# Kernel tuning notes

Measured on AMD Instinct MI355X. Metric: run time of the kernel, lower is better.

## Reference

```python
import jax, jax.numpy as jnp
import numpy as np

B, LATENT, P, NUM_ATOMS, H, L, E = 16, 128, 16, 64, 64, 4, 32768
N = P * NUM_ATOMS  # 1024

def _lin(k, i, o, s=0.05):
    kw, kb = jax.random.split(k)
    return jax.random.normal(kw, (i, o), jnp.float32) * s, jax.random.normal(kb, (o,), jnp.float32) * s

def setup_inputs() -> dict:
    key = jax.random.key(0)
    ks = jax.random.split(key, 32)
    z = jax.random.normal(ks[0], (B, LATENT), jnp.float32)
    edge_index = jax.random.randint(ks[1], (2, E), 0, N, jnp.int32)
    # build_node_features: (frame/P, atom/num_atoms, 1) per node
    fr = jnp.repeat(jnp.arange(P), NUM_ATOMS) / P
    at = jnp.tile(jnp.arange(NUM_ATOMS), P) / NUM_ATOMS
    node_features = jnp.stack([fr, at, jnp.ones(N)], -1).astype(jnp.float32)
    Wg, bg = _lin(ks[2], LATENT, H)
    Wn, bn = _lin(ks[3], 3, H)
    def stack(fn, base):
        outs = [fn(jax.random.fold_in(key, base + l)) for l in range(L)]
        return tuple(jnp.stack(t) for t in zip(*outs))
    eW1, eb1 = stack(lambda k: _lin(k, 2 * H + 1, H), 100)
    eW2, eb2 = stack(lambda k: _lin(k, H, H), 200)
    cW1, cb1 = stack(lambda k: _lin(k, H, H), 300)
    cW2 = jnp.stack([jax.random.normal(jax.random.fold_in(key, 400 + l), (H, 1), jnp.float32) * 0.05 for l in range(L)])
    nW1, nb1 = stack(lambda k: _lin(k, 2 * H, H), 500)
    nW2, nb2 = stack(lambda k: _lin(k, H, H), 600)
    lng = jnp.ones((L, H), jnp.float32)
    lnb = jnp.zeros((L, H), jnp.float32)
    oW1, ob1 = _lin(ks[4], H, H)
    oW2, ob2 = _lin(ks[5], H, 3)
    return dict(z=z, edge_index=edge_index, node_features=node_features, Wg=Wg, bg=bg, Wn=Wn, bn=bn,
                eW1=eW1, eb1=eb1, eW2=eW2, eb2=eb2, cW1=cW1, cb1=cb1, cW2=cW2,
                nW1=nW1, nb1=nb1, nW2=nW2, nb2=nb2, lng=lng, lnb=lnb,
                oW1=oW1, ob1=ob1, oW2=oW2, ob2=ob2)

def _forward(z, edge_index, node_features, Wg, bg, Wn, bn, eW1, eb1, eW2, eb2,
             cW1, cb1, cW2, nW1, nb1, nW2, nb2, lng, lnb, oW1, ob1, oW2, ob2):
    b = z.shape[0]
    n = node_features.shape[0]
    row, col = edge_index[0], edge_index[1]  # aggregate messages to row
    counts = jnp.clip(jnp.zeros((n,), jnp.float32).at[row].add(1.0), 1.0, None)
    g = z @ Wg + bg                              # [B,H]
    h = (node_features @ Wn + bn)[None] + g[:, None]  # [B,N,H]
    pos = jnp.zeros((b, n, 3), h.dtype)
    for l in range(L):
        hi, hj = h[:, row], h[:, col]            # [B,E,H] gathers
        diff = pos[:, row] - pos[:, col]         # [B,E,3]
        d2 = jnp.sum(diff * diff, -1, keepdims=True)
        m = jax.nn.silu(jnp.concatenate([hi, hj, d2], -1) @ eW1[l] + eb1[l])
        m = jax.nn.silu(m @ eW2[l] + eb2[l])     # [B,E,H]
        w = jax.nn.silu(m @ cW1[l] + cb1[l]) @ cW2[l]  # [B,E,1]
        trans = diff * w
        pos = pos + jnp.zeros_like(pos).at[:, row].add(trans) / counts[None, :, None]
        agg = jnp.zeros_like(h).at[:, row].add(m)      # scatter-sum to nodes
        u = jax.nn.silu(jnp.concatenate([h, agg], -1) @ nW1[l] + nb1[l]) @ nW2[l] + nb2[l]
        h = h + u                                 # node residual
        mu = jnp.mean(h, -1, keepdims=True)
        var = jnp.mean((h - mu) ** 2, -1, keepdims=True)
        h = (h - mu) * jax.lax.rsqrt(var + 1e-5) * lng[l] + lnb[l]
    out = jax.nn.relu(h @ oW1 + ob1) @ oW2 + ob2   # [B,N,3]
    return out.reshape(b, -1)

def reference(z, edge_index, node_features, Wg, bg, Wn, bn, eW1, eb1, eW2, eb2,
              cW1, cb1, cW2, nW1, nb1, nW2, nb2, lng, lnb, oW1, ob1, oW2, ob2):
    return _forward(z, edge_index, node_features, Wg, bg, Wn, bn, eW1, eb1, eW2, eb2,
                    cW1, cb1, cW2, nW1, nb1, nW2, nb2, lng, lnb, oW1, ob1, oW2, ob2)
```

## Files before the change

kernel.cpp:

```cpp
#include <hip/hip_runtime.h>
#include <hip/hip_bf16.h>


namespace {

constexpr int kE = 32768, kLat = 128;

typedef __attribute__((ext_vector_type(8))) short short8;
typedef __attribute__((ext_vector_type(4))) float floatx4;

__device__ __forceinline__ unsigned short f2bf(float f){
  union { float f; unsigned int u; } v; v.f = f;
  unsigned int r = v.u + 0x7fffu + ((v.u >> 16) & 1u);
  return (unsigned short)(r >> 16);
}
__device__ __forceinline__ unsigned int packbf(float a, float b){
  return ((unsigned int)f2bf(b) << 16) | (unsigned int)f2bf(a);
}
__device__ __forceinline__ unsigned int pack2f(float a, float b){
  unsigned int ua = __float_as_uint(a) + 0x8000u;
  unsigned int ub = __float_as_uint(b) + 0x8000u;
  return __builtin_amdgcn_perm(ub, ua, 0x07060302);
}
__device__ __forceinline__ float bflo(unsigned int u){
  union { unsigned int u; float f; } v; v.u = u << 16; return v.f;
}
__device__ __forceinline__ float bfhi(unsigned int u){
  union { unsigned int u; float f; } v; v.u = u & 0xffff0000u; return v.f;
}
__device__ __forceinline__ float silu2(float x){
  float u = __builtin_amdgcn_exp2f(-1.44269504f * x);
  return x * __builtin_amdgcn_rcpf(1.0f + u);
}

__device__ __forceinline__ void stage16k(float* Wl, const float* src, int tid){
  const float4* p = (const float4*)src;
  float4* d = (float4*)Wl;
  d[tid]       = p[tid];
  d[tid + 256] = p[tid + 256];
  d[tid + 512] = p[tid + 512];
  d[tid + 768] = p[tid + 768];
}
__device__ __forceinline__ void xtwrite(float* XTl, int j0, int r0,
                                        const float v[4][4]){
  #pragma unroll
  for (int j = 0; j < 4; j++){
    float4 t = { v[0][j], v[1][j], v[2][j], v[3][j] };
    *(float4*)(XTl + (j0 + j)*68 + r0) = t;
  }
}
__device__ __forceinline__ void gemm64(const float* Wl, const float* XTl,
                                       int j0, int r0, float acc[4][4]){
  #pragma unroll 4
  for (int k = 0; k < 64; k++){
    float4 w = *(const float4*)(Wl + k*64 + j0);
    float4 x = *(const float4*)(XTl + k*68 + r0);
    float xv[4] = { x.x, x.y, x.z, x.w };
    float wv[4] = { w.x, w.y, w.z, w.w };
    #pragma unroll
    for (int i = 0; i < 4; i++)
      #pragma unroll
      for (int j = 0; j < 4; j++)
        acc[i][j] += xv[i]*wv[j];
  }
}

__global__ void k_scancnt(const int* ei, int* off, int* fill){
  __shared__ int s0[1024];
  __shared__ int s1[1024];
  int t = threadIdx.x;
  s0[t] = 0; fill[t] = 0;
  __syncthreads();
  #pragma unroll
  for (int i = 0; i < 32; i++) atomicAdd(&s0[ei[i*1024 + t]], 1);
  __syncthreads();
  int c = s0[t];
  int* src = s0; int* dst = s1;
  for (int o = 1; o < 1024; o <<= 1){
    int v = src[t] + ((t >= o) ? src[t-o] : 0);
    dst[t] = v; __syncthreads();
    int* tmp = src; src = dst; dst = tmp;
  }
  int inc = src[t];
  off[t] = inc - c;
  if (t == 1023) off[1024] = inc;
}

__global__ void k_bucket(const int* ei, const int* off, int* fill, int* ecol,
                         const float* eW2, unsigned short* wfragE,
                         const float* z, const float* Wg, const float* bg,
                         float* g){
  int e = blockIdx.x*256 + threadIdx.x;
  int r = ei[e];
  int s = atomicAdd(&fill[r], 1);
  ecol[off[r] + s] = ei[kE + e];
  if (blockIdx.x < 4){
    int l = blockIdx.x;
    for (int i = threadIdx.x; i < 4096; i += 256){
      int f = i >> 9, lane = (i >> 3) & 63, j8 = i & 7;
      int jt = f >> 1, ks = f & 1;
      int k = ks*32 + (lane >> 4)*8 + j8;
      int j = jt*16 + (lane & 15);
      wfragE[l*4096 + i] = f2bf(eW2[l*4096 + k*64 + j]);
    }
  } else if (blockIdx.x < 8){
    int b = (blockIdx.x - 4)*4 + (threadIdx.x >> 6);
    int j = threadIdx.x & 63;
    float acc = bg[j];
    for (int k = 0; k < kLat; k++) acc += z[b*kLat + k] * Wg[k*64 + j];
    g[b*64 + j] = acc;
  }
}

__global__ __launch_bounds__(256, 1) void k_preA(const float* nf, const float* Wn,
      const float* bn, const float* g, const float* eW1, const float* eb1,
      float* An1, float* An2, float* Ag1, float* Ag2){
  __shared__ __align__(16) float W0[4096];
  __shared__ __align__(16) float W1[4096];
  __shared__ __align__(16) float HR[16*68];
  int tid = threadIdx.x;
  if (blockIdx.x == 64){
    int bb = tid >> 4, j0 = (tid & 15)*4;
    float a1[4] = {0.f,0.f,0.f,0.f}, a2[4] = {0.f,0.f,0.f,0.f};
    for (int k = 0; k < 64; k++){
      float gk = g[bb*64 + k];
      float4 w1 = *(const float4*)(eW1 + k*64 + j0);
      float4 w2 = *(const float4*)(eW1 + 4096 + k*64 + j0);
      a1[0] += gk*w1.x; a1[1] += gk*w1.y; a1[2] += gk*w1.z; a1[3] += gk*w1.w;
      a2[0] += gk*w2.x; a2[1] += gk*w2.y; a2[2] += gk*w2.z; a2[3] += gk*w2.w;
    }
    float4 o1 = { a1[0], a1[1], a1[2], a1[3] };
    float4 o2 = { a2[0], a2[1], a2[2], a2[3] };
    *(float4*)(Ag1 + bb*64 + j0) = o1;
    *(float4*)(Ag2 + bb*64 + j0) = o2;
    return;
  }
  {
    const float4* e1a = (const float4*)(eW1);
    const float4* e1b = (const float4*)(eW1 + 4096);
    for (int i = tid; i < 1024; i += 256){
      ((float4*)W0)[i] = e1a[i]; ((float4*)W1)[i] = e1b[i];
    }
  }
  int rl = tid >> 4, c = tid & 15, j0 = c*4;
  int n = blockIdx.x*16 + rl;
  float f0 = nf[n*3], f1 = nf[n*3+1], f2 = nf[n*3+2];
  float4 hv;
  hv.x = f0*Wn[j0+0] + f1*Wn[64+j0+0] + f2*Wn[128+j0+0] + bn[j0+0];
  hv.y = f0*Wn[j0+1] + f1*Wn[64+j0+1] + f2*Wn[128+j0+1] + bn[j0+1];
  hv.z = f0*Wn[j0+2] + f1*Wn[64+j0+2] + f2*Wn[128+j0+2] + bn[j0+2];
  hv.w = f0*Wn[j0+3] + f1*Wn[64+j0+3] + f2*Wn[128+j0+3] + bn[j0+3];
  *(float4*)(HR + rl*68 + j0) = hv;
  __syncthreads();
  float4 b1 = *(const float4*)(eb1 + j0);
  float a1[4] = { b1.x, b1.y, b1.z, b1.w };
  float a2[4] = { 0.f, 0.f, 0.f, 0.f };
  #pragma unroll 8
  for (int k = 0; k < 64; k++){
    float hk = HR[rl*68 + k];
    float4 w1 = *(const float4*)(W0 + k*64 + j0);
    float4 w2 = *(const float4*)(W1 + k*64 + j0);
    a1[0] += hk*w1.x; a1[1] += hk*w1.y; a1[2] += hk*w1.z; a1[3] += hk*w1.w;
    a2[0] += hk*w2.x; a2[1] += hk*w2.y; a2[2] += hk*w2.z; a2[3] += hk*w2.w;
  }
  float4 o1 = { a1[0], a1[1], a1[2], a1[3] };
  float4 o2 = { a2[0], a2[1], a2[2], a2[3] };
  *(float4*)(An1 + n*64 + j0) = o1;
  *(float4*)(An2 + n*64 + j0) = o2;
}

__global__ __launch_bounds__(256, 1) void k_pre1(const float* nf, const float* Wn,
      const float* bn, const float* g, const float* An1, const float* An2,
      const float* Ag1, const float* Ag2, float* h, float* A1,
      unsigned short* A2){
  int idx = blockIdx.x*256 + threadIdx.x;
  int row = idx >> 4;
  int j0  = (idx & 15) * 4;
  int n = row >> 4, bb = row & 15;
  float4 a1 = *(const float4*)(An1 + n*64 + j0);
  float4 g1 = *(const float4*)(Ag1 + bb*64 + j0);
  a1.x += g1.x; a1.y += g1.y; a1.z += g1.z; a1.w += g1.w;
  *(float4*)(A1 + row*64 + j0) = a1;
  float4 a2 = *(const float4*)(An2 + n*64 + j0);
  float4 g2 = *(const float4*)(Ag2 + bb*64 + j0);
  a2.x += g2.x; a2.y += g2.y; a2.z += g2.z; a2.w += g2.w;
  uint2 pk; pk.x = packbf(a2.x, a2.y); pk.y = packbf(a2.z, a2.w);
  *(uint2*)(A2 + row*64 + j0) = pk;
  float f0 = nf[n*3], f1 = nf[n*3+1], f2 = nf[n*3+2];
  float4 w0 = *(const float4*)(Wn + j0);
  float4 w1 = *(const float4*)(Wn + 64 + j0);
  float4 w2 = *(const float4*)(Wn + 128 + j0);
  float4 bv = *(const float4*)(bn + j0);
  float4 gv = *(const float4*)(g + bb*64 + j0);
  float4 hv;
  hv.x = f0*w0.x + f1*w1.x + f2*w2.x + bv.x + gv.x;
  hv.y = f0*w0.y + f1*w1.y + f2*w2.y + bv.y + gv.y;
  hv.z = f0*w0.z + f1*w1.z + f2*w2.z + bv.z + gv.z;
  hv.w = f0*w0.w + f1*w1.w + f2*w2.w + bv.w + gv.w;
  *(float4*)(h + (bb*1024 + n)*64 + j0) = hv;
}

template <bool LAST>
__global__ __launch_bounds__(256) void k_layer(int l,
      const float* A1r, const unsigned short* A2r,
      float* A1w, unsigned short* A2w,
      float* h, const unsigned short* wfragE, const float* eb2,
      const int* off, const int* ecol,
      const float* nW1, const float* nb1_, const float* nW2, const float* nb2_,
      const float* lng_, const float* lnb_, const float* eW1, const float* eb1_,
      const float* oW1, const float* ob1_, const float* oW2, const float* ob2_,
      float* out){
  __shared__ __align__(16) float W[4096];
  __shared__ __align__(16) float XT[64*68];
  __shared__ __align__(16) float AGL[64*68];
  __shared__ float W2o[192];
  __shared__ float ob2s[4];
  int tid = threadIdx.x, bid = blockIdx.x;
  int n0 = bid * 4;
  int lane = tid & 63, wv = tid >> 6, m = lane & 15, quad = lane >> 4;

  {
    int nd = n0 + wv;
    short8 wf[8];
    #pragma unroll
    for (int f = 0; f < 8; f++)
      wf[f] = *(const short8*)(wfragE + l*4096 + f*512 + lane*8);
    floatx4 dini[4], agg[4];
    #pragma unroll
    for (int jt = 0; jt < 4; jt++){
      dini[jt] = *(const floatx4*)(eb2 + l*64 + jt*16 + quad*4);
      agg[jt] = (floatx4){0.f,0.f,0.f,0.f};
    }
    int e0 = off[nd], e1 = off[nd+1];
    if (e0 < e1){
      float4 a1[4];
      #pragma unroll
      for (int ks = 0; ks < 2; ks++){
        a1[ks*2+0] = *(const float4*)(A1r + (nd<<10) + (m<<6) + ks*32 + quad*8);
        a1[ks*2+1] = *(const float4*)(A1r + (nd<<10) + (m<<6) + ks*32 + quad*8 + 4);
      }
      int c0 = ecol[e0];
      uint4 p0 = *(const uint4*)(A2r + ((c0<<4)+m)*64 + quad*8);
      uint4 p1 = *(const uint4*)(A2r + ((c0<<4)+m)*64 + 32 + quad*8);
      for (int e = e0; e < e1; e++){
        uint4 c_0 = p0, c_1 = p1;
        if (e + 1 < e1){
          int cn = ecol[e+1];
          p0 = *(const uint4*)(A2r + ((cn<<4)+m)*64 + quad*8);
          p1 = *(const uint4*)(A2r + ((cn<<4)+m)*64 + 32 + quad*8);
        }
        short8 bfr[2];
        #pragma unroll
        for (int ks = 0; ks < 2; ks++){
          uint4 a2r = (ks == 0) ? c_0 : c_1;
          float4 x0 = a1[ks*2+0];
          float4 x1 = a1[ks*2+1];
          float v0 = silu2(x0.x + bflo(a2r.x));
          float v1 = silu2(x0.y + bfhi(a2r.x));
          float v2 = silu2(x0.z + bflo(a2r.y));
          float v3 = silu2(x0.w + bfhi(a2r.y));
          float v4 = silu2(x1.x + bflo(a2r.z));
          float v5 = silu2(x1.y + bfhi(a2r.z));
          float v6 = silu2(x1.z + bflo(a2r.w));
          float v7 = silu2(x1.w + bfhi(a2r.w));
          union { uint4 u; short8 s; } bu;
          bu.u.x = pack2f(v0, v1); bu.u.y = pack2f(v2, v3);
          bu.u.z = pack2f(v4, v5); bu.u.w = pack2f(v6, v7);
          bfr[ks] = bu.s;
        }
        #pragma unroll
        for (int jt = 0; jt < 4; jt++){
          floatx4 d = dini[jt];
          d = __builtin_amdgcn_mfma_f32_16x16x32_bf16(wf[jt*2+0], bfr[0], d, 0, 0, 0);
          d = __builtin_amdgcn_mfma_f32_16x16x32_bf16(wf[jt*2+1], bfr[1], d, 0, 0, 0);
          floatx4 a = agg[jt];
          a.x += silu2(d.x); a.y += silu2(d.y);
          a.z += silu2(d.z); a.w += silu2(d.w);
          agg[jt] = a;
        }
      }
    }
    #pragma unroll
    for (int jt = 0; jt < 4; jt++){
      #pragma unroll
      for (int i = 0; i < 4; i++)
        AGL[(jt*16 + quad*4 + i)*68 + wv*16 + m] = agg[jt][i];
    }
  }

  int c = tid & 15, gq = tid >> 4;
  int j0 = c*4, r0 = gq*4;

  stage16k(W, nW1 + l*8192, tid);
  float hold[4][4];
  #pragma unroll
  for (int i = 0; i < 4; i++){
    int rr = r0 + i;
    int n = n0 + (rr >> 4), bb = rr & 15;
    float4 v = *(const float4*)(h + (bb*1024 + n)*64 + j0);
    hold[i][0]=v.x; hold[i][1]=v.y; hold[i][2]=v.z; hold[i][3]=v.w;
  }
  xtwrite(XT, j0, r0, hold);
  float acc[4][4];
  { float4 b1 = *(const float4*)(nb1_ + l*64 + j0);
    float bv[4] = { b1.x, b1.y, b1.z, b1.w };
    #pragma unroll
    for (int i = 0; i < 4; i++)
      #pragma unroll
      for (int j = 0; j < 4; j++) acc[i][j] = bv[j]; }
  __syncthreads();
  gemm64(W, XT, j0, r0, acc);
  __syncthreads();
  stage16k(W, nW1 + l*8192 + 4096, tid);
  __syncthreads();
  gemm64(W, AGL, j0, r0, acc);
  #pragma unroll
  for (int i = 0; i < 4; i++)
    #pragma unroll
    for (int j = 0; j < 4; j++) acc[i][j] = silu2(acc[i][j]);
  __syncthreads();
  stage16k(W, nW2 + l*4096, tid);
  xtwrite(XT, j0, r0, acc);
  float u[4][4];
  { float4 b2 = *(const float4*)(nb2_ + l*64 + j0);
    float bv[4] = { b2.x, b2.y, b2.z, b2.w };
    #pragma unroll
    for (int i = 0; i < 4; i++)
      #pragma unroll
      for (int j = 0; j < 4; j++) u[i][j] = bv[j]; }
  __syncthreads();
  gemm64(W, XT, j0, r0, u);
  float4 lgv = *(const float4*)(lng_ + l*64 + j0);
  float4 lbv = *(const float4*)(lnb_ + l*64 + j0);
  float hn[4][4];
  #pragma unroll
  for (int i = 0; i < 4; i++){
    float hv[4];
    #pragma unroll
    for (int j = 0; j < 4; j++) hv[j] = hold[i][j] + u[i][j];
    float s1 = hv[0]+hv[1]+hv[2]+hv[3];
    float s2 = hv[0]*hv[0]+hv[1]*hv[1]+hv[2]*hv[2]+hv[3]*hv[3];
    s1 += __shfl_xor(s1, 1, 64); s1 += __shfl_xor(s1, 2, 64);
    s1 += __shfl_xor(s1, 4, 64); s1 += __shfl_xor(s1, 8, 64);
    s2 += __shfl_xor(s2, 1, 64); s2 += __shfl_xor(s2, 2, 64);
    s2 += __shfl_xor(s2, 4, 64); s2 += __shfl_xor(s2, 8, 64);
    float mu  = s1 * (1.0f/64.0f);
    float var = s2 * (1.0f/64.0f) - mu*mu;
    float rs  = rsqrtf(var + 1e-5f);
    hn[i][0] = (hv[0]-mu)*rs*lgv.x + lbv.x;
    hn[i][1] = (hv[1]-mu)*rs*lgv.y + lbv.y;
    hn[i][2] = (hv[2]-mu)*rs*lgv.z + lbv.z;
    hn[i][3] = (hv[3]-mu)*rs*lgv.w + lbv.w;
  }

  if (!LAST){
    #pragma unroll
    for (int i = 0; i < 4; i++){
      int rr = r0 + i;
      int n = n0 + (rr >> 4), bb = rr & 15;
      float4 v = { hn[i][0], hn[i][1], hn[i][2], hn[i][3] };
      *(float4*)(h + (bb*1024 + n)*64 + j0) = v;
    }
    __syncthreads();
    stage16k(W, eW1 + (l+1)*8256, tid);
    xtwrite(XT, j0, r0, hn);
    float a1r[4][4];
    { float4 b1 = *(const float4*)(eb1_ + (l+1)*64 + j0);
      float bv[4] = { b1.x, b1.y, b1.z, b1.w };
      #pragma unroll
      for (int i = 0; i < 4; i++)
        #pragma unroll
        for (int j = 0; j < 4; j++) a1r[i][j] = bv[j]; }
    __syncthreads();
    gemm64(W, XT, j0, r0, a1r);
    __syncthreads();
    stage16k(W, eW1 + (l+1)*8256 + 4096, tid);
    float a2r[4][4];
    #pragma unroll
    for (int i = 0; i < 4; i++)
      #pragma unroll
      for (int j = 0; j < 4; j++) a2r[i][j] = 0.f;
    __syncthreads();
    gemm64(W, XT, j0, r0, a2r);
    #pragma unroll
    for (int i = 0; i < 4; i++){
      int rr = r0 + i;
      int n = n0 + (rr >> 4), bb = rr & 15;
      int tb = (n*16 + bb)*64 + j0;
      float4 o1 = { a1r[i][0], a1r[i][1], a1r[i][2], a1r[i][3] };
      *(float4*)(A1w + tb) = o1;
      uint2 pk; pk.x = packbf(a2r[i][0], a2r[i][1]);
      pk.y = packbf(a2r[i][2], a2r[i][3]);
      *(uint2*)(A2w + tb) = pk;
    }
  } else {
    __syncthreads();
    stage16k(W, oW1, tid);
    if (tid < 192) W2o[tid] = oW2[tid];
    if (tid < 3)   ob2s[tid] = ob2_[tid];
    xtwrite(XT, j0, r0, hn);
    __syncthreads();
    float tr[4][4];
    { float4 b1 = *(const float4*)(ob1_ + j0);
      float bv[4] = { b1.x, b1.y, b1.z, b1.w };
      #pragma unroll
      for (int i = 0; i < 4; i++)
        #pragma unroll
        for (int j = 0; j < 4; j++) tr[i][j] = bv[j]; }
    gemm64(W, XT, j0, r0, tr);
    #pragma unroll
    for (int i = 0; i < 4; i++)
      #pragma unroll
      for (int j = 0; j < 4; j++) tr[i][j] = fmaxf(tr[i][j], 0.f);
    float po[4][3];
    #pragma unroll
    for (int i = 0; i < 4; i++){ po[i][0]=0.f; po[i][1]=0.f; po[i][2]=0.f; }
    #pragma unroll
    for (int j = 0; j < 4; j++){
      float w0 = W2o[(j0+j)*3 + 0];
      float w1 = W2o[(j0+j)*3 + 1];
      float w2 = W2o[(j0+j)*3 + 2];
      #pragma unroll
      for (int i = 0; i < 4; i++){
        po[i][0] += tr[i][j]*w0;
        po[i][1] += tr[i][j]*w1;
        po[i][2] += tr[i][j]*w2;
      }
    }
    #pragma unroll
    for (int i = 0; i < 4; i++)
      #pragma unroll
      for (int uu = 0; uu < 3; uu++){
        float v = po[i][uu];
        v += __shfl_xor(v, 1, 64); v += __shfl_xor(v, 2, 64);
        v += __shfl_xor(v, 4, 64); v += __shfl_xor(v, 8, 64);
        po[i][uu] = v;
      }
    if (c == 0){
      #pragma unroll
      for (int i = 0; i < 4; i++){
        int rr = r0 + i;
        int n = n0 + (rr >> 4), bb = rr & 15;
        out[bb*3072 + n*3 + 0] = po[i][0] + ob2s[0];
        out[bb*3072 + n*3 + 1] = po[i][1] + ob2s[1];
        out[bb*3072 + n*3 + 2] = po[i][2] + ob2s[2];
      }
    }
  }
}

}

extern "C" void kernel_launch(void* const* d_in, const int* in_sizes, int n_in,
                              void* d_out, int out_size, void* d_ws, size_t ws_size,
                              hipStream_t stream){
  const float* z   = (const float*)d_in[0];
  const int*   ei  = (const int*)d_in[1];
  const float* nf  = (const float*)d_in[2];
  const float* Wg  = (const float*)d_in[3];  const float* bg  = (const float*)d_in[4];
  const float* Wn  = (const float*)d_in[5];  const float* bn  = (const float*)d_in[6];
  const float* eW1 = (const float*)d_in[7];  const float* eb1 = (const float*)d_in[8];
  const float* eW2 = (const float*)d_in[9];  const float* eb2 = (const float*)d_in[10];
  const float* nW1 = (const float*)d_in[14]; const float* nb1 = (const float*)d_in[15];
  const float* nW2 = (const float*)d_in[16]; const float* nb2 = (const float*)d_in[17];
  const float* lng = (const float*)d_in[18]; const float* lnb = (const float*)d_in[19];
  const float* oW1 = (const float*)d_in[20]; const float* ob1 = (const float*)d_in[21];
  const float* oW2 = (const float*)d_in[22]; const float* ob2 = (const float*)d_in[23];

  float* W      = (float*)d_ws;
  float* h      = W;
  float* A1a    = W + 1048576;
  float* A1b    = W + 2097152;
  unsigned short* A2a    = (unsigned short*)(W + 3145728);
  unsigned short* A2b    = (unsigned short*)(W + 3670016);
  unsigned short* wfragE = (unsigned short*)(W + 4194304);
  float* g      = W + 4202496;
  float* An1    = W + 4203520;
  float* An2    = W + 4269056;
  float* Ag1    = W + 4334592;
  float* Ag2    = W + 4335616;
  int*   off    = (int*)(W + 4336640);
  int*   fill   = off + 1025;
  int*   ecol   = fill + 1024;

  k_scancnt<<<1, 1024, 0, stream>>>(ei, off, fill);
  k_bucket <<<128, 256, 0, stream>>>(ei, off, fill, ecol, eW2, wfragE, z, Wg, bg, g);
  k_preA   <<<65,  256, 0, stream>>>(nf, Wn, bn, g, eW1, eb1, An1, An2, Ag1, Ag2);
  k_pre1   <<<1024,256, 0, stream>>>(nf, Wn, bn, g, An1, An2, Ag1, Ag2, h, A1a, A2a);

  for (int l = 0; l < 4; l++){
    const float* A1r = (l & 1) ? A1b : A1a;
    const unsigned short* A2r = (l & 1) ? A2b : A2a;
    float* A1w = (l & 1) ? A1a : A1b;
    unsigned short* A2w = (l & 1) ? A2a : A2b;
    if (l < 3)
      k_layer<false><<<256, 256, 0, stream>>>(l, A1r, A2r, A1w, A2w, h, wfragE,
            eb2, off, ecol, nW1, nb1, nW2, nb2, lng, lnb, eW1, eb1,
            oW1, ob1, oW2, ob2, (float*)d_out);
    else
      k_layer<true> <<<256, 256, 0, stream>>>(l, A1r, A2r, A1w, A2w, h, wfragE,
            eb2, off, ecol, nW1, nb1, nW2, nb2, lng, lnb, eW1, eb1,
            oW1, ob1, oW2, ob2, (float*)d_out);
  }
}
```

Measured before the change: 336.2 us.

## Split layer kernel into 512 blocks with warp-specialised weight staging and merged preprocessing

The layer kernel now processes 2 nodes per block instead of 4, doubling the grid to 512 blocks. Two waves share each node's edge list, interleaving edges and combining partial aggregates with shared-memory atomics. The block is split into 128 compute threads that run the node MLP GEMMs and 128 threads that prefetch the next weight tile into double-buffered LDS, so weight staging overlaps the GEMMs. Separately, the preA kernel is merged into k_bucket and the g computation into k_scancnt, removing one launch. The costs are half the threads idle during compute, LDS atomics, and larger shared memory per block.

```diff
diff --git a/kernel.cpp b/kernel.cpp
--- a/kernel.cpp
+++ b/kernel.cpp
@@ -33,28 +33,18 @@
   return x * __builtin_amdgcn_rcpf(1.0f + u);
 }
 
-__device__ __forceinline__ void stage16k(float* Wl, const float* src, int tid){
+__device__ __forceinline__ void stageU(float* Wl, const float* src, int u){
   const float4* p = (const float4*)src;
   float4* d = (float4*)Wl;
-  d[tid]       = p[tid];
-  d[tid + 256] = p[tid + 256];
-  d[tid + 512] = p[tid + 512];
-  d[tid + 768] = p[tid + 768];
-}
-__device__ __forceinline__ void xtwrite(float* XTl, int j0, int r0,
-                                        const float v[4][4]){
   #pragma unroll
-  for (int j = 0; j < 4; j++){
-    float4 t = { v[0][j], v[1][j], v[2][j], v[3][j] };
-    *(float4*)(XTl + (j0 + j)*68 + r0) = t;
-  }
-}
-__device__ __forceinline__ void gemm64(const float* Wl, const float* XTl,
+  for (int q = 0; q < 8; q++) d[u + q*128] = p[u + q*128];
+}
+__device__ __forceinline__ void gemm32(const float* Wl, const float* Xl,
                                        int j0, int r0, float acc[4][4]){
   #pragma unroll 4
   for (int k = 0; k < 64; k++){
     float4 w = *(const float4*)(Wl + k*64 + j0);
-    float4 x = *(const float4*)(XTl + k*68 + r0);
+    float4 x = *(const float4*)(Xl + k*36 + r0);
     float xv[4] = { x.x, x.y, x.z, x.w };
     float wv[4] = { w.x, w.y, w.z, w.w };
     #pragma unroll
@@ -65,7 +55,9 @@
   }
 }
 
-__global__ void k_scancnt(const int* ei, int* off, int* fill){
+__global__ void k_scancnt(const int* ei, int* off, int* fill,
+                          const float* z, const float* Wg, const float* bg,
+                          float* g){
   __shared__ int s0[1024];
   __shared__ int s1[1024];
   int t = threadIdx.x;
@@ -84,42 +76,66 @@
   int inc = src[t];
   off[t] = inc - c;
   if (t == 1023) off[1024] = inc;
+  int b = t >> 6, j = t & 63;
+  float acc = bg[j];
+  for (int k = 0; k < kLat; k++) acc += z[b*kLat + k] * Wg[k*64 + j];
+  g[b*64 + j] = acc;
 }
 
 __global__ void k_bucket(const int* ei, const int* off, int* fill, int* ecol,
                          const float* eW2, unsigned short* wfragE,
-                         const float* z, const float* Wg, const float* bg,
-                         float* g){
-  int e = blockIdx.x*256 + threadIdx.x;
+                         const float* nf, const float* Wn, const float* bn,
+                         const float* eW1, const float* eb1, const float* g,
+                         float* An1, float* An2, float* Ag1, float* Ag2){
+  __shared__ __align__(16) float W0[4096];
+  __shared__ __align__(16) float W1[4096];
+  __shared__ __align__(16) float HR[16*68];
+  int tid = threadIdx.x, bid = blockIdx.x;
+  int e = bid*256 + tid;
   int r = ei[e];
   int s = atomicAdd(&fill[r], 1);
   ecol[off[r] + s] = ei[kE + e];
-  if (blockIdx.x < 4){
-    int l = blockIdx.x;
-    for (int i = threadIdx.x; i < 4096; i += 256){
+  if (bid < 4){
+    int l = bid;
+    for (int i = tid; i < 4096; i += 256){
       int f = i >> 9, lane = (i >> 3) & 63, j8 = i & 7;
       int jt = f >> 1, ks = f & 1;
       int k = ks*32 + (lane >> 4)*8 + j8;
       int j = jt*16 + (lane & 15);
       wfragE[l*4096 + i] = f2bf(eW2[l*4096 + k*64 + j]);
     }
-  } else if (blockIdx.x < 8){
-    int b = (blockIdx.x - 4)*4 + (threadIdx.x >> 6);
-    int j = threadIdx.x & 63;
-    float acc = bg[j];
-    for (int k = 0; k < kLat; k++) acc += z[b*kLat + k] * Wg[k*64 + j];
-    g[b*64 + j] = acc;
-  }
-}
-
-__global__ __launch_bounds__(256, 1) void k_preA(const float* nf, const float* Wn,
-      const float* bn, const float* g, const float* eW1, const float* eb1,
-      float* An1, float* An2, float* Ag1, float* Ag2){
-  __shared__ __align__(16) float W0[4096];
-  __shared__ __align__(16) float W1[4096];
-  __shared__ __align__(16) float HR[16*68];
-  int tid = threadIdx.x;
-  if (blockIdx.x == 64){
+  } else if (bid < 68){
+    const float4* e1a = (const float4*)(eW1);
+    const float4* e1b = (const float4*)(eW1 + 4096);
+    for (int i = tid; i < 1024; i += 256){
+      ((float4*)W0)[i] = e1a[i]; ((float4*)W1)[i] = e1b[i];
+    }
+    int rl = tid >> 4, c = tid & 15, j0 = c*4;
+    int n = (bid - 4)*16 + rl;
+    float f0 = nf[n*3], f1 = nf[n*3+1], f2 = nf[n*3+2];
+    float4 hv;
+    hv.x = f0*Wn[j0+0] + f1*Wn[64+j0+0] + f2*Wn[128+j0+0] + bn[j0+0];
+    hv.y = f0*Wn[j0+1] + f1*Wn[64+j0+1] + f2*Wn[128+j0+1] + bn[j0+1];
+    hv.z = f0*Wn[j0+2] + f1*Wn[64+j0+2] + f2*Wn[128+j0+2] + bn[j0+2];
+    hv.w = f0*Wn[j0+3] + f1*Wn[64+j0+3] + f2*Wn[128+j0+3] + bn[j0+3];
+    *(float4*)(HR + rl*68 + j0) = hv;
+    __syncthreads();
+    float4 b1 = *(const float4*)(eb1 + j0);
+    float a1[4] = { b1.x, b1.y, b1.z, b1.w };
+    float a2[4] = { 0.f, 0.f, 0.f, 0.f };
+    #pragma unroll 8
+    for (int k = 0; k < 64; k++){
+      float hk = HR[rl*68 + k];
+      float4 w1 = *(const float4*)(W0 + k*64 + j0);
+      float4 w2 = *(const float4*)(W1 + k*64 + j0);
+      a1[0] += hk*w1.x; a1[1] += hk*w1.y; a1[2] += hk*w1.z; a1[3] += hk*w1.w;
+      a2[0] += hk*w2.x; a2[1] += hk*w2.y; a2[2] += hk*w2.z; a2[3] += hk*w2.w;
+    }
+    float4 o1 = { a1[0], a1[1], a1[2], a1[3] };
+    float4 o2 = { a2[0], a2[1], a2[2], a2[3] };
+    *(float4*)(An1 + n*64 + j0) = o1;
+    *(float4*)(An2 + n*64 + j0) = o2;
+  } else if (bid == 68){
     int bb = tid >> 4, j0 = (tid & 15)*4;
     float a1[4] = {0.f,0.f,0.f,0.f}, a2[4] = {0.f,0.f,0.f,0.f};
     for (int k = 0; k < 64; k++){
@@ -133,40 +149,7 @@
     float4 o2 = { a2[0], a2[1], a2[2], a2[3] };
     *(float4*)(Ag1 + bb*64 + j0) = o1;
     *(float4*)(Ag2 + bb*64 + j0) = o2;
-    return;
-  }
-  {
-    const float4* e1a = (const float4*)(eW1);
-    const float4* e1b = (const float4*)(eW1 + 4096);
-    for (int i = tid; i < 1024; i += 256){
-      ((float4*)W0)[i] = e1a[i]; ((float4*)W1)[i] = e1b[i];
-    }
-  }
-  int rl = tid >> 4, c = tid & 15, j0 = c*4;
-  int n = blockIdx.x*16 + rl;
-  float f0 = nf[n*3], f1 = nf[n*3+1], f2 = nf[n*3+2];
-  float4 hv;
-  hv.x = f0*Wn[j0+0] + f1*Wn[64+j0+0] + f2*Wn[128+j0+0] + bn[j0+0];
-  hv.y = f0*Wn[j0+1] + f1*Wn[64+j0+1] + f2*Wn[128+j0+1] + bn[j0+1];
-  hv.z = f0*Wn[j0+2] + f1*Wn[64+j0+2] + f2*Wn[128+j0+2] + bn[j0+2];
-  hv.w = f0*Wn[j0+3] + f1*Wn[64+j0+3] + f2*Wn[128+j0+3] + bn[j0+3];
-  *(float4*)(HR + rl*68 + j0) = hv;
-  __syncthreads();
-  float4 b1 = *(const float4*)(eb1 + j0);
-  float a1[4] = { b1.x, b1.y, b1.z, b1.w };
-  float a2[4] = { 0.f, 0.f, 0.f, 0.f };
-  #pragma unroll 8
-  for (int k = 0; k < 64; k++){
-    float hk = HR[rl*68 + k];
-    float4 w1 = *(const float4*)(W0 + k*64 + j0);
-    float4 w2 = *(const float4*)(W1 + k*64 + j0);
-    a1[0] += hk*w1.x; a1[1] += hk*w1.y; a1[2] += hk*w1.z; a1[3] += hk*w1.w;
-    a2[0] += hk*w2.x; a2[1] += hk*w2.y; a2[2] += hk*w2.z; a2[3] += hk*w2.w;
-  }
-  float4 o1 = { a1[0], a1[1], a1[2], a1[3] };
-  float4 o2 = { a2[0], a2[1], a2[2], a2[3] };
-  *(float4*)(An1 + n*64 + j0) = o1;
-  *(float4*)(An2 + n*64 + j0) = o2;
+  }
 }
 
 __global__ __launch_bounds__(256, 1) void k_pre1(const float* nf, const float* Wn,
@@ -210,17 +193,21 @@
       const float* lng_, const float* lnb_, const float* eW1, const float* eb1_,
       const float* oW1, const float* ob1_, const float* oW2, const float* ob2_,
       float* out){
-  __shared__ __align__(16) float W[4096];
-  __shared__ __align__(16) float XT[64*68];
-  __shared__ __align__(16) float AGL[64*68];
+  __shared__ __align__(16) float Wa[4096];
+  __shared__ __align__(16) float Wb[4096];
+  __shared__ __align__(16) float XT[64*36];
+  __shared__ __align__(16) float AGL[64*36];
   __shared__ float W2o[192];
   __shared__ float ob2s[4];
   int tid = threadIdx.x, bid = blockIdx.x;
-  int n0 = bid * 4;
+  int n0 = bid * 2;
   int lane = tid & 63, wv = tid >> 6, m = lane & 15, quad = lane >> 4;
 
+  for (int i = tid; i < 64*36; i += 256) AGL[i] = 0.f;
+  __syncthreads();
+
   {
-    int nd = n0 + wv;
+    int nd = n0 + (wv >> 1);
     short8 wf[8];
     #pragma unroll
     for (int f = 0; f < 8; f++)
@@ -231,7 +218,7 @@
       dini[jt] = *(const floatx4*)(eb2 + l*64 + jt*16 + quad*4);
       agg[jt] = (floatx4){0.f,0.f,0.f,0.f};
     }
-    int e0 = off[nd], e1 = off[nd+1];
+    int e0 = off[nd] + (wv & 1), e1 = off[nd+1];
     if (e0 < e1){
       float4 a1[4];
       #pragma unroll
@@ -242,10 +229,10 @@
       int c0 = ecol[e0];
       uint4 p0 = *(const uint4*)(A2r + ((c0<<4)+m)*64 + quad*8);
       uint4 p1 = *(const uint4*)(A2r + ((c0<<4)+m)*64 + 32 + quad*8);
-      for (int e = e0; e < e1; e++){
+      for (int e = e0; e < e1; e += 2){
         uint4 c_0 = p0, c_1 = p1;
-        if (e + 1 < e1){
-          int cn = ecol[e+1];
+        if (e + 2 < e1){
+          int cn = ecol[e+2];
           p0 = *(const uint4*)(A2r + ((cn<<4)+m)*64 + quad*8);
           p1 = *(const uint4*)(A2r + ((cn<<4)+m)*64 + 32 + quad*8);
         }
@@ -280,170 +267,198 @@
         }
       }
     }
-    #pragma unroll
-    for (int jt = 0; jt < 4; jt++){
+    int rloc = (wv >> 1)*16 + m;
+    #pragma unroll
+    for (int jt = 0; jt < 4; jt++)
       #pragma unroll
       for (int i = 0; i < 4; i++)
-        AGL[(jt*16 + quad*4 + i)*68 + wv*16 + m] = agg[jt][i];
-    }
-  }
-
+        atomicAdd(&AGL[(jt*16 + quad*4 + i)*36 + rloc], agg[jt][i]);
+  }
+
+  bool lo = (tid < 128);
+  int up = tid - 128;
   int c = tid & 15, gq = tid >> 4;
   int j0 = c*4, r0 = gq*4;
 
-  stage16k(W, nW1 + l*8192, tid);
   float hold[4][4];
-  #pragma unroll
-  for (int i = 0; i < 4; i++){
-    int rr = r0 + i;
-    int n = n0 + (rr >> 4), bb = rr & 15;
-    float4 v = *(const float4*)(h + (bb*1024 + n)*64 + j0);
-    hold[i][0]=v.x; hold[i][1]=v.y; hold[i][2]=v.z; hold[i][3]=v.w;
-  }
-  xtwrite(XT, j0, r0, hold);
   float acc[4][4];
-  { float4 b1 = *(const float4*)(nb1_ + l*64 + j0);
-    float bv[4] = { b1.x, b1.y, b1.z, b1.w };
-    #pragma unroll
-    for (int i = 0; i < 4; i++)
-      #pragma unroll
-      for (int j = 0; j < 4; j++) acc[i][j] = bv[j]; }
-  __syncthreads();
-  gemm64(W, XT, j0, r0, acc);
-  __syncthreads();
-  stage16k(W, nW1 + l*8192 + 4096, tid);
-  __syncthreads();
-  gemm64(W, AGL, j0, r0, acc);
-  #pragma unroll
-  for (int i = 0; i < 4; i++)
-    #pragma unroll
-    for (int j = 0; j < 4; j++) acc[i][j] = silu2(acc[i][j]);
-  __syncthreads();
-  stage16k(W, nW2 + l*4096, tid);
-  xtwrite(XT, j0, r0, acc);
-  float u[4][4];
-  { float4 b2 = *(const float4*)(nb2_ + l*64 + j0);
-    float bv[4] = { b2.x, b2.y, b2.z, b2.w };
-    #pragma unroll
-    for (int i = 0; i < 4; i++)
-      #pragma unroll
-      for (int j = 0; j < 4; j++) u[i][j] = bv[j]; }
-  __syncthreads();
-  gemm64(W, XT, j0, r0, u);
-  float4 lgv = *(const float4*)(lng_ + l*64 + j0);
-  float4 lbv = *(const float4*)(lnb_ + l*64 + j0);
-  float hn[4][4];
-  #pragma unroll
-  for (int i = 0; i < 4; i++){
-    float hv[4];
-    #pragma unroll
-    for (int j = 0; j < 4; j++) hv[j] = hold[i][j] + u[i][j];
-    float s1 = hv[0]+hv[1]+hv[2]+hv[3];
-    float s2 = hv[0]*hv[0]+hv[1]*hv[1]+hv[2]*hv[2]+hv[3]*hv[3];
-    s1 += __shfl_xor(s1, 1, 64); s1 += __shfl_xor(s1, 2, 64);
-    s1 += __shfl_xor(s1, 4, 64); s1 += __shfl_xor(s1, 8, 64);
-    s2 += __shfl_xor(s2, 1, 64); s2 += __shfl_xor(s2, 2, 64);
-    s2 += __shfl_xor(s2, 4, 64); s2 += __shfl_xor(s2, 8, 64);
-    float mu  = s1 * (1.0f/64.0f);
-    float var = s2 * (1.0f/64.0f) - mu*mu;
-    float rs  = rsqrtf(var + 1e-5f);
-    hn[i][0] = (hv[0]-mu)*rs*lgv.x + lbv.x;
-    hn[i][1] = (hv[1]-mu)*rs*lgv.y + lbv.y;
-    hn[i][2] = (hv[2]-mu)*rs*lgv.z + lbv.z;
-    hn[i][3] = (hv[3]-mu)*rs*lgv.w + lbv.w;
-  }
-
-  if (!LAST){
+  if (lo){
     #pragma unroll
     for (int i = 0; i < 4; i++){
       int rr = r0 + i;
-      int n = n0 + (rr >> 4), bb = rr & 15;
-      float4 v = { hn[i][0], hn[i][1], hn[i][2], hn[i][3] };
-      *(float4*)(h + (bb*1024 + n)*64 + j0) = v;
-    }
-    __syncthreads();
-    stage16k(W, eW1 + (l+1)*8256, tid);
-    xtwrite(XT, j0, r0, hn);
-    float a1r[4][4];
-    { float4 b1 = *(const float4*)(eb1_ + (l+1)*64 + j0);
-      float bv[4] = { b1.x, b1.y, b1.z, b1.w };
-      #pragma unroll
-      for (int i = 0; i < 4; i++)
-        #pragma unroll
-        for (int j = 0; j < 4; j++) a1r[i][j] = bv[j]; }
-    __syncthreads();
-    gemm64(W, XT, j0, r0, a1r);
-    __syncthreads();
-    stage16k(W, eW1 + (l+1)*8256 + 4096, tid);
-    float a2r[4][4];
+      int nd2 = n0 + (rr >> 4), bb = rr & 15;
+      float4 v = *(const float4*)(h + (bb*1024 + nd2)*64 + j0);
+      hold[i][0]=v.x; hold[i][1]=v.y; hold[i][2]=v.z; hold[i][3]=v.w;
+    }
+    #pragma unroll
+    for (int j = 0; j < 4; j++){
+      float4 t = { hold[0][j], hold[1][j], hold[2][j], hold[3][j] };
+      *(float4*)(XT + (j0 + j)*36 + r0) = t;
+    }
+    float4 b1 = *(const float4*)(nb1_ + l*64 + j0);
+    float bv[4] = { b1.x, b1.y, b1.z, b1.w };
     #pragma unroll
     for (int i = 0; i < 4; i++)
       #pragma unroll
-      for (int j = 0; j < 4; j++) a2r[i][j] = 0.f;
-    __syncthreads();
-    gemm64(W, XT, j0, r0, a2r);
+      for (int j = 0; j < 4; j++) acc[i][j] = bv[j];
+  } else {
+    stageU(Wa, nW1 + l*8192, up);
+  }
+  __syncthreads();
+  if (lo) gemm32(Wa, XT, j0, r0, acc);
+  else    stageU(Wb, nW1 + l*8192 + 4096, up);
+  __syncthreads();
+  if (lo){
+    gemm32(Wb, AGL, j0, r0, acc);
+    #pragma unroll
+    for (int i = 0; i < 4; i++)
+      #pragma unroll
+      for (int j = 0; j < 4; j++) acc[i][j] = silu2(acc[i][j]);
+    #pragma unroll
+    for (int j = 0; j < 4; j++){
+      float4 t = { acc[0][j], acc[1][j], acc[2][j], acc[3][j] };
+      *(float4*)(XT + (j0 + j)*36 + r0) = t;
+    }
+  } else {
+    stageU(Wa, nW2 + l*4096, up);
+  }
+  __syncthreads();
+  float hn[4][4];
+  if (lo){
+    float u4[4][4];
+    float4 b2 = *(const float4*)(nb2_ + l*64 + j0);
+    float bv[4] = { b2.x, b2.y, b2.z, b2.w };
+    #pragma unroll
+    for (int i = 0; i < 4; i++)
+      #pragma unroll
+      for (int j = 0; j < 4; j++) u4[i][j] = bv[j];
+    gemm32(Wa, XT, j0, r0, u4);
+    float4 lgv = *(const float4*)(lng_ + l*64 + j0);
+    float4 lbv = *(const float4*)(lnb_ + l*64 + j0);
     #pragma unroll
     for (int i = 0; i < 4; i++){
-      int rr = r0 + i;
-      int n = n0 + (rr >> 4), bb = rr & 15;
-      int tb = (n*16 + bb)*64 + j0;
-      float4 o1 = { a1r[i][0], a1r[i][1], a1r[i][2], a1r[i][3] };
-      *(float4*)(A1w + tb) = o1;
-      uint2 pk; pk.x = packbf(a2r[i][0], a2r[i][1]);
-      pk.y = packbf(a2r[i][2], a2r[i][3]);
-      *(uint2*)(A2w + tb) = pk;
-    }
-  } else {
-    __syncthreads();
-    stage16k(W, oW1, tid);
-    if (tid < 192) W2o[tid] = oW2[tid];
-    if (tid < 3)   ob2s[tid] = ob2_[tid];
-    xtwrite(XT, j0, r0, hn);
-    __syncthreads();
-    float tr[4][4];
-    { float4 b1 = *(const float4*)(ob1_ + j0);
-      float bv[4] = { b1.x, b1.y, b1.z, b1.w };
-      #pragma unroll
-      for (int i = 0; i < 4; i++)
-        #pragma unroll
-        for (int j = 0; j < 4; j++) tr[i][j] = bv[j]; }
-    gemm64(W, XT, j0, r0, tr);
-    #pragma unroll
-    for (int i = 0; i < 4; i++)
-      #pragma unroll
-      for (int j = 0; j < 4; j++) tr[i][j] = fmaxf(tr[i][j], 0.f);
-    float po[4][3];
-    #pragma unroll
-    for (int i = 0; i < 4; i++){ po[i][0]=0.f; po[i][1]=0.f; po[i][2]=0.f; }
-    #pragma unroll
-    for (int j = 0; j < 4; j++){
-      float w0 = W2o[(j0+j)*3 + 0];
-      float w1 = W2o[(j0+j)*3 + 1];
-      float w2 = W2o[(j0+j)*3 + 2];
-      #pragma unroll
-      for (int i = 0; i < 4; i++){
-        po[i][0] += tr[i][j]*w0;
-        po[i][1] += tr[i][j]*w1;
-        po[i][2] += tr[i][j]*w2;
-      }
-    }
-    #pragma unroll
-    for (int i = 0; i < 4; i++)
-      #pragma unroll
-      for (int uu = 0; uu < 3; uu++){
-        float v = po[i][uu];
-        v += __shfl_xor(v, 1, 64); v += __shfl_xor(v, 2, 64);
-        v += __shfl_xor(v, 4, 64); v += __shfl_xor(v, 8, 64);
-        po[i][uu] = v;
-      }
-    if (c == 0){
+      float hv[4];
+      #pragma unroll
+      for (int j = 0; j < 4; j++) hv[j] = hold[i][j] + u4[i][j];
+      float s1 = hv[0]+hv[1]+hv[2]+hv[3];
+      float s2 = hv[0]*hv[0]+hv[1]*hv[1]+hv[2]*hv[2]+hv[3]*hv[3];
+      s1 += __shfl_xor(s1, 1, 64); s1 += __shfl_xor(s1, 2, 64);
+      s1 += __shfl_xor(s1, 4, 64); s1 += __shfl_xor(s1, 8, 64);
+      s2 += __shfl_xor(s2, 1, 64); s2 += __shfl_xor(s2, 2, 64);
+      s2 += __shfl_xor(s2, 4, 64); s2 += __shfl_xor(s2, 8, 64);
+      float mu  = s1 * (1.0f/64.0f);
+      float var = s2 * (1.0f/64.0f) - mu*mu;
+      float rs  = rsqrtf(var + 1e-5f);
+      hn[i][0] = (hv[0]-mu)*rs*lgv.x + lbv.x;
+      hn[i][1] = (hv[1]-mu)*rs*lgv.y + lbv.y;
+      hn[i][2] = (hv[2]-mu)*rs*lgv.z + lbv.z;
+      hn[i][3] = (hv[3]-mu)*rs*lgv.w + lbv.w;
+    }
+    if (!LAST){
       #pragma unroll
       for (int i = 0; i < 4; i++){
         int rr = r0 + i;
-        int n = n0 + (rr >> 4), bb = rr & 15;
-        out[bb*3072 + n*3 + 0] = po[i][0] + ob2s[0];
-        out[bb*3072 + n*3 + 1] = po[i][1] + ob2s[1];
-        out[bb*3072 + n*3 + 2] = po[i][2] + ob2s[2];
+        int nd2 = n0 + (rr >> 4), bb = rr & 15;
+        float4 v = { hn[i][0], hn[i][1], hn[i][2], hn[i][3] };
+        *(float4*)(h + (bb*1024 + nd2)*64 + j0) = v;
+      }
+    }
+    #pragma unroll
+    for (int j = 0; j < 4; j++){
+      float4 t = { hn[0][j], hn[1][j], hn[2][j], hn[3][j] };
+      *(float4*)(AGL + (j0 + j)*36 + r0) = t;
+    }
+  } else {
+    if (!LAST){
+      stageU(Wb, eW1 + (l+1)*8256, up);
+    } else {
+      stageU(Wb, oW1, up);
+      W2o[up] = oW2[up];
+      if (up < 64) W2o[128 + up] = oW2[128 + up];
+      if (up < 3)  ob2s[up] = ob2_[up];
+    }
+  }
+  __syncthreads();
+  if (!LAST){
+    float a1r[4][4];
+    if (lo){
+      float4 b1 = *(const float4*)(eb1_ + (l+1)*64 + j0);
+      float bv[4] = { b1.x, b1.y, b1.z, b1.w };
+      #pragma unroll
+      for (int i = 0; i < 4; i++)
+        #pragma unroll
+        for (int j = 0; j < 4; j++) a1r[i][j] = bv[j];
+      gemm32(Wb, AGL, j0, r0, a1r);
+    } else {
+      stageU(Wa, eW1 + (l+1)*8256 + 4096, up);
+    }
+    __syncthreads();
+    if (lo){
+      float a2r[4][4];
+      #pragma unroll
+      for (int i = 0; i < 4; i++)
+        #pragma unroll
+        for (int j = 0; j < 4; j++) a2r[i][j] = 0.f;
+      gemm32(Wa, AGL, j0, r0, a2r);
+      #pragma unroll
+      for (int i = 0; i < 4; i++){
+        int rr = r0 + i;
+        int nd2 = n0 + (rr >> 4), bb = rr & 15;
+        int tb = (nd2*16 + bb)*64 + j0;
+        float4 o1 = { a1r[i][0], a1r[i][1], a1r[i][2], a1r[i][3] };
+        *(float4*)(A1w + tb) = o1;
+        uint2 pk; pk.x = packbf(a2r[i][0], a2r[i][1]);
+        pk.y = packbf(a2r[i][2], a2r[i][3]);
+        *(uint2*)(A2w + tb) = pk;
+      }
+    }
+  } else {
+    if (lo){
+      float tr[4][4];
+      float4 b1 = *(const float4*)(ob1_ + j0);
+      float bv[4] = { b1.x, b1.y, b1.z, b1.w };
+      #pragma unroll
+      for (int i = 0; i < 4; i++)
+        #pragma unroll
+        for (int j = 0; j < 4; j++) tr[i][j] = bv[j];
+      gemm32(Wb, AGL, j0, r0, tr);
+      #pragma unroll
+      for (int i = 0; i < 4; i++)
+        #pragma unroll
+        for (int j = 0; j < 4; j++) tr[i][j] = fmaxf(tr[i][j], 0.f);
+      float po[4][3];
+      #pragma unroll
+      for (int i = 0; i < 4; i++){ po[i][0]=0.f; po[i][1]=0.f; po[i][2]=0.f; }
+      #pragma unroll
+      for (int j = 0; j < 4; j++){
+        float w0 = W2o[(j0+j)*3 + 0];
+        float w1 = W2o[(j0+j)*3 + 1];
+        float w2 = W2o[(j0+j)*3 + 2];
+        #pragma unroll
+        for (int i = 0; i < 4; i++){
+          po[i][0] += tr[i][j]*w0;
+          po[i][1] += tr[i][j]*w1;
+          po[i][2] += tr[i][j]*w2;
+        }
+      }
+      #pragma unroll
+      for (int i = 0; i < 4; i++)
+        #pragma unroll
+        for (int uu = 0; uu < 3; uu++){
+          float v = po[i][uu];
+          v += __shfl_xor(v, 1, 64); v += __shfl_xor(v, 2, 64);
+          v += __shfl_xor(v, 4, 64); v += __shfl_xor(v, 8, 64);
+          po[i][uu] = v;
+        }
+      if (c == 0){
+        #pragma unroll
+        for (int i = 0; i < 4; i++){
+          int rr = r0 + i;
+          int nd2 = n0 + (rr >> 4), bb = rr & 15;
+          out[bb*3072 + nd2*3 + 0] = po[i][0] + ob2s[0];
+          out[bb*3072 + nd2*3 + 1] = po[i][1] + ob2s[1];
+          out[bb*3072 + nd2*3 + 2] = po[i][2] + ob2s[2];
+        }
       }
     }
   }
@@ -483,9 +498,9 @@
   int*   fill   = off + 1025;
   int*   ecol   = fill + 1024;
 
-  k_scancnt<<<1, 1024, 0, stream>>>(ei, off, fill);
-  k_bucket <<<128, 256, 0, stream>>>(ei, off, fill, ecol, eW2, wfragE, z, Wg, bg, g);
-  k_preA   <<<65,  256, 0, stream>>>(nf, Wn, bn, g, eW1, eb1, An1, An2, Ag1, Ag2);
+  k_scancnt<<<1, 1024, 0, stream>>>(ei, off, fill, z, Wg, bg, g);
+  k_bucket <<<128, 256, 0, stream>>>(ei, off, fill, ecol, eW2, wfragE,
+                                     nf, Wn, bn, eW1, eb1, g, An1, An2, Ag1, Ag2);
   k_pre1   <<<1024,256, 0, stream>>>(nf, Wn, bn, g, An1, An2, Ag1, Ag2, h, A1a, A2a);
 
   for (int l = 0; l < 4; l++){
@@ -494,11 +509,11 @@
     float* A1w = (l & 1) ? A1a : A1b;
     unsigned short* A2w = (l & 1) ? A2a : A2b;
     if (l < 3)
-      k_layer<false><<<256, 256, 0, stream>>>(l, A1r, A2r, A1w, A2w, h, wfragE,
+      k_layer<false><<<512, 256, 0, stream>>>(l, A1r, A2r, A1w, A2w, h, wfragE,
             eb2, off, ecol, nW1, nb1, nW2, nb2, lng, lnb, eW1, eb1,
             oW1, ob1, oW2, ob2, (float*)d_out);
     else
-      k_layer<true> <<<256, 256, 0, stream>>>(l, A1r, A2r, A1w, A2w, h, wfragE,
+      k_layer<true> <<<512, 256, 0, stream>>>(l, A1r, A2r, A1w, A2w, h, wfragE,
             eb2, off, ecol, nW1, nb1, nW2, nb2, lng, lnb, eW1, eb1,
             oW1, ob1, oW2, ob2, (float*)d_out);
   }
```

Result: no change. 335.1 us (median of 2 runs) (-0.3%).
